# Performance work log

Hardware: AMD Instinct MI355X
Metric: run time of the kernel (lower is better)

Reference implementation:

```python
import jax, jax.numpy as jnp
import numpy as np

B, C, H, W = 256, 2, 152, 272   # flow map: 2-channel, 152x272 (608x1088 / 4)
K = 500                          # max tracked objects per image
ID_RANGE = 20000                 # pool of unique track ids per batch element


def setup_inputs() -> dict:
    key = jax.random.key(0)
    k1, k2, k3, k4, k5, k6, k7 = jax.random.split(key, 7)
    flow = jax.random.normal(k1, (B, C, H, W), dtype=jnp.float32)
    mask = (jax.random.uniform(k2, (B, K)) < 0.5).astype(jnp.float32)
    index = jax.random.randint(k3, (B, K), 0, H * W, dtype=jnp.int32)
    # ids: unique nonzero track ids per batch element (matches real tracker data)
    ids = jax.vmap(
        lambda k: jax.random.permutation(k, jnp.arange(1, ID_RANGE + 1, dtype=jnp.int32))[:K]
    )(jax.random.split(k4, B))
    ids2 = jax.vmap(jax.random.permutation)(jax.random.split(k5, B), ids)
    drop = jax.random.uniform(k6, (B, K))
    ids2 = jnp.where(drop < 0.2, 0, jnp.where(drop > 0.85, ids2 + 100000, ids2))
    index2 = jax.random.randint(k7, (B, K), 0, H * W, dtype=jnp.int32)
    return dict(flow=flow, mask=mask, index=index, ids=ids, index2=index2, ids2=ids2)


def reference(flow, mask, index, ids, index2, ids2):
    Bn, Cn, Hn, Wn = flow.shape
    Kn = index.shape[1]
    # _tranpose_and_gather_feat: [B,C,H,W] -> [B,H*W,C] -> gather along dim 1
    feat = jnp.transpose(flow, (0, 2, 3, 1)).reshape(Bn, Hn * Wn, Cn)
    idx = jnp.broadcast_to(index[:, :, None].astype(jnp.int32), (Bn, Kn, Cn))
    pred = jnp.take_along_axis(feat, idx, axis=1)                 # [B,K,2]
    xy = pred * mask[:, :, None]                                   # [B,K,2]

    # Vectorized ID join: for each j, first position x in ids[b] with ids[b,x]==ids2[b,j]
    match = ids[:, :, None] == ids2[:, None, :]                    # [B,K(x),K(j)] bool
    found = jnp.any(match, axis=1)                                 # [B,K(j)]
    xpos = jnp.argmax(match, axis=1)                               # first match index
    valid = found & (ids2 != 0)

    # target coords decoded from flattened index2 (faithful: true division by 272)
    vals = jnp.stack(
        [(index2 % 272).astype(jnp.float32), index2.astype(jnp.float32) / 272.0],
        axis=-1,
    )                                                              # [B,K,2]

    # Scatter via a padded row (invalid -> slot K, then sliced off)
    tgt = jnp.where(valid, xpos, Kn)                               # [B,K]
    bidx = jnp.arange(Bn)[:, None]
    reordered = jnp.zeros((Bn, Kn + 1, 2), jnp.float32).at[bidx, tgt].set(vals)[:, :Kn]
    mask_index = jnp.zeros((Bn, Kn + 1), jnp.float32).at[bidx, tgt].set(1.0)[:, :Kn]

    xy = xy * mask_index[:, :, None]
    # torch mask was expanded to [B,K,2] before .sum() -> factor 2
    denom = 2.0 * jnp.sum(mask) + 0.0001
    return jnp.sum(jnp.abs(xy - reordered)) / denom
```

## Files before the change

### kernel.cpp

```cpp
#include <hip/hip_runtime.h>

#define Bn   256
#define Kn   500
#define Wn   272
#define HWn  (152 * 272)
#define TABLE 1024


__global__ __launch_bounds__(256) void join_loss_kernel(
    const float* __restrict__ flow, const float* __restrict__ mask,
    const int* __restrict__ index, const int* __restrict__ ids,
    const int* __restrict__ index2, const int* __restrict__ ids2,
    float* __restrict__ partials ) {
  const int b = blockIdx.x;
  const int tid = threadIdx.x;
  __shared__ int h_key[TABLE];
  __shared__ int h_val[TABLE];

  int  v2a = ids2[b * Kn + tid];
  int  i2a = index2[b * Kn + tid];
  int  ida = ids[b * Kn + tid];
  float ma = mask[b * Kn + tid];
  int  hwa = index[b * Kn + tid];
  const bool hasB = (tid + 256) < Kn;
  int  v2b = 0, i2b = 0, idb = 0, hwb = 0;
  float mb = 0.f;
  if (hasB) {
    v2b = ids2[b * Kn + tid + 256];
    i2b = index2[b * Kn + tid + 256];
    idb = ids[b * Kn + tid + 256];
    mb  = mask[b * Kn + tid + 256];
    hwb = index[b * Kn + tid + 256];
  }

  for (int i = tid; i < TABLE; i += 256) h_key[i] = 0;
  __syncthreads();

  #pragma unroll
  for (int s = 0; s < 2; ++s) {
    int v  = s ? v2b : v2a;
    int i2 = s ? i2b : i2a;
    if (v != 0 && (s == 0 || hasB)) {
      unsigned h = (((unsigned)v * 2654435761u) >> 22) & (TABLE - 1);
      while (true) {
        int old = atomicCAS(&h_key[h], 0, v);
        if (old == 0) { h_val[h] = i2; break; }
        if (old == v) break;
        h = (h + 1) & (TABLE - 1);
      }
    }
  }
  __syncthreads();

  float lloss = 0.f, lmask = ma + mb;
  #pragma unroll
  for (int s = 0; s < 2; ++s) {
    if (s && !hasB) break;
    int id  = s ? idb : ida;
    float m = s ? mb : ma;
    int  hw = s ? hwb : hwa;
    unsigned h = (((unsigned)id * 2654435761u) >> 22) & (TABLE - 1);
    int i2 = -1;
    while (true) {
      int k = h_key[h];
      if (k == 0) break;
      if (k == id) { i2 = h_val[h]; break; }
      h = (h + 1) & (TABLE - 1);
    }
    if (i2 >= 0) {
      float p0 = flow[(size_t)(b * 2 + 0) * HWn + hw] * m;
      float p1 = flow[(size_t)(b * 2 + 1) * HWn + hw] * m;
      lloss += fabsf(p0 - (float)(i2 % Wn)) + fabsf(p1 - (float)i2 / 272.0f);
    }
  }

  for (int off = 32; off; off >>= 1) {
    lloss += __shfl_down(lloss, off, 64);
    lmask += __shfl_down(lmask, off, 64);
  }
  __shared__ float s_l[4], s_m[4];
  const int wave = tid >> 6, lane = tid & 63;
  if (lane == 0) { s_l[wave] = lloss; s_m[wave] = lmask; }
  __syncthreads();
  if (tid == 0) {
    partials[b]       = s_l[0] + s_l[1] + s_l[2] + s_l[3];
    partials[256 + b] = s_m[0] + s_m[1] + s_m[2] + s_m[3];
  }
}

__global__ __launch_bounds__(64) void finalize_kernel(
    const float* __restrict__ partials, float* __restrict__ out) {
  const int lane = threadIdx.x;
  float l = 0.f, m = 0.f;
  #pragma unroll
  for (int i = 0; i < 4; ++i) {
    l += partials[lane + 64 * i];
    m += partials[256 + lane + 64 * i];
  }
  for (int off = 32; off; off >>= 1) {
    l += __shfl_down(l, off, 64);
    m += __shfl_down(m, off, 64);
  }
  if (lane == 0) out[0] = l / (2.0f * m + 0.0001f);
}

extern "C" void kernel_launch(void* const* d_in, const int* in_sizes, int n_in,
                              void* d_out, int out_size, void* d_ws, size_t ws_size,
                              hipStream_t stream) {
  const float* flow   = (const float*)d_in[0];
  const float* mask   = (const float*)d_in[1];
  const int*   index  = (const int*)d_in[2];
  const int*   ids    = (const int*)d_in[3];
  const int*   index2 = (const int*)d_in[4];
  const int*   ids2   = (const int*)d_in[5];
  float* partials = (float*)d_ws;
  join_loss_kernel<<<Bn, 256, 0, stream>>>(flow, mask, index, ids, index2, ids2, partials);
  finalize_kernel<<<1, 64, 0, stream>>>(partials, (float*)d_out);
}
```

Before: 120.9 us.

## Use one thread per object, prefetch flow gathers, and enlarge hash table

The block grows from 256 to 512 threads so each thread handles a single object instead of two. The flow gathers are now issued before the hash build rather than after the lookup, so their latency overlaps the table build. The shared hash table doubles to 2048 slots to reduce probe chains. In exchange, every thread now loads flow even for unmatched entries, and larger blocks with more shared memory may reduce occupancy.

```diff
diff --git a/kernel.cpp b/kernel.cpp
--- a/kernel.cpp
+++ b/kernel.cpp
@@ -4,62 +4,55 @@
 #define Kn   500
 #define Wn   272
 #define HWn  (152 * 272)
-#define TABLE 1024
+#define TABLE 2048
 
 
-__global__ __launch_bounds__(256) void join_loss_kernel(
+__global__ __launch_bounds__(512) void join_loss_kernel(
     const float* __restrict__ flow, const float* __restrict__ mask,
     const int* __restrict__ index, const int* __restrict__ ids,
     const int* __restrict__ index2, const int* __restrict__ ids2,
     float* __restrict__ partials ) {
   const int b = blockIdx.x;
   const int tid = threadIdx.x;
+  const bool act = tid < Kn;
   __shared__ int h_key[TABLE];
   __shared__ int h_val[TABLE];
 
-  int  v2a = ids2[b * Kn + tid];
-  int  i2a = index2[b * Kn + tid];
-  int  ida = ids[b * Kn + tid];
-  float ma = mask[b * Kn + tid];
-  int  hwa = index[b * Kn + tid];
-  const bool hasB = (tid + 256) < Kn;
-  int  v2b = 0, i2b = 0, idb = 0, hwb = 0;
-  float mb = 0.f;
-  if (hasB) {
-    v2b = ids2[b * Kn + tid + 256];
-    i2b = index2[b * Kn + tid + 256];
-    idb = ids[b * Kn + tid + 256];
-    mb  = mask[b * Kn + tid + 256];
-    hwb = index[b * Kn + tid + 256];
+  int   v2 = 0, i2v = 0, id = 0, hw = 0;
+  float m = 0.f;
+  if (act) {
+    v2  = ids2[b * Kn + tid];
+    i2v = index2[b * Kn + tid];
+    id  = ids[b * Kn + tid];
+    m   = mask[b * Kn + tid];
+    hw  = index[b * Kn + tid];
+  }
+  float p0 = 0.f, p1 = 0.f;
+  if (act) {
+    p0 = flow[(size_t)(b * 2 + 0) * HWn + hw];
+    p1 = flow[(size_t)(b * 2 + 1) * HWn + hw];
   }
 
-  for (int i = tid; i < TABLE; i += 256) h_key[i] = 0;
+  h_key[tid]        = 0;
+  h_key[tid + 512]  = 0;
+  h_key[tid + 1024] = 0;
+  h_key[tid + 1536] = 0;
   __syncthreads();
 
-  #pragma unroll
-  for (int s = 0; s < 2; ++s) {
-    int v  = s ? v2b : v2a;
-    int i2 = s ? i2b : i2a;
-    if (v != 0 && (s == 0 || hasB)) {
-      unsigned h = (((unsigned)v * 2654435761u) >> 22) & (TABLE - 1);
-      while (true) {
-        int old = atomicCAS(&h_key[h], 0, v);
-        if (old == 0) { h_val[h] = i2; break; }
-        if (old == v) break;
-        h = (h + 1) & (TABLE - 1);
-      }
+  if (v2 != 0) {
+    unsigned h = (((unsigned)v2 * 2654435761u) >> 21) & (TABLE - 1);
+    while (true) {
+      int old = atomicCAS(&h_key[h], 0, v2);
+      if (old == 0) { h_val[h] = i2v; break; }
+      if (old == v2) break;
+      h = (h + 1) & (TABLE - 1);
     }
   }
   __syncthreads();
 
-  float lloss = 0.f, lmask = ma + mb;
-  #pragma unroll
-  for (int s = 0; s < 2; ++s) {
-    if (s && !hasB) break;
-    int id  = s ? idb : ida;
-    float m = s ? mb : ma;
-    int  hw = s ? hwb : hwa;
-    unsigned h = (((unsigned)id * 2654435761u) >> 22) & (TABLE - 1);
+  float lloss = 0.f, lmask = m;
+  if (act) {
+    unsigned h = (((unsigned)id * 2654435761u) >> 21) & (TABLE - 1);
     int i2 = -1;
     while (true) {
       int k = h_key[h];
@@ -68,9 +61,8 @@
       h = (h + 1) & (TABLE - 1);
     }
     if (i2 >= 0) {
-      float p0 = flow[(size_t)(b * 2 + 0) * HWn + hw] * m;
-      float p1 = flow[(size_t)(b * 2 + 1) * HWn + hw] * m;
-      lloss += fabsf(p0 - (float)(i2 % Wn)) + fabsf(p1 - (float)i2 / 272.0f);
+      lloss = fabsf(p0 * m - (float)(i2 % Wn)) +
+              fabsf(p1 * m - (float)i2 / 272.0f);
     }
   }
 
@@ -78,13 +70,16 @@
     lloss += __shfl_down(lloss, off, 64);
     lmask += __shfl_down(lmask, off, 64);
   }
-  __shared__ float s_l[4], s_m[4];
+  __shared__ float s_l[8], s_m[8];
   const int wave = tid >> 6, lane = tid & 63;
   if (lane == 0) { s_l[wave] = lloss; s_m[wave] = lmask; }
   __syncthreads();
   if (tid == 0) {
-    partials[b]       = s_l[0] + s_l[1] + s_l[2] + s_l[3];
-    partials[256 + b] = s_m[0] + s_m[1] + s_m[2] + s_m[3];
+    float L = 0.f, M = 0.f;
+    #pragma unroll
+    for (int i = 0; i < 8; ++i) { L += s_l[i]; M += s_m[i]; }
+    partials[b]       = L;
+    partials[256 + b] = M;
   }
 }
 
@@ -114,6 +109,6 @@
   const int*   index2 = (const int*)d_in[4];
   const int*   ids2   = (const int*)d_in[5];
   float* partials = (float*)d_ws;
-  join_loss_kernel<<<Bn, 256, 0, stream>>>(flow, mask, index, ids, index2, ids2, partials);
+  join_loss_kernel<<<Bn, 512, 0, stream>>>(flow, mask, index, ids, index2, ids2, partials);
   finalize_kernel<<<1, 64, 0, stream>>>(partials, (float*)d_out);
 }
```

Measured after the change: 120.5 us. About the same (-0.3%).
